# Optimization experiments

Measured on AMD Instinct MI355X. Metric: run time of the kernel, lower is better.

The kernel has to match this reference:

```python
import jax, jax.numpy as jnp
import numpy as np

N_NODES = 100000
DIM = 64
N_EDGES = 1250000
PRESERVE = 0.1  # preserve_ratio in GCN module


def gcn_conv(x, W, b, row, col, edge_w, num_nodes):
    """PyG GCNConv with normalize=True: symmetric norm with added self-loops.
    x: [N, d], W: [d, d_out], edge (row -> col) with weight edge_w: [E].
    """
    # add self-loops with weight 1
    loop = jnp.arange(num_nodes, dtype=row.dtype)
    r = jnp.concatenate([row, loop])
    c = jnp.concatenate([col, loop])
    w = jnp.concatenate([edge_w, jnp.ones((num_nodes,), dtype=edge_w.dtype)])
    # symmetric degree normalization: deg computed at target (col)
    deg = jax.ops.segment_sum(w, c, num_segments=num_nodes)
    dinv = jnp.where(deg > 0, jax.lax.rsqrt(deg), 0.0)
    norm = dinv[r] * w * dinv[c]  # [E+N]
    xw = x @ W  # [N, d_out] (linear transform before propagation)
    msg = xw[r] * norm[:, None]  # gather + scale
    out = jax.ops.segment_sum(msg, c, num_segments=num_nodes)  # scatter-add at targets
    return out + b


def setup_inputs() -> dict:
    key = jax.random.key(0)
    ks = jax.random.split(key, 8)
    skill_embed = jax.random.normal(ks[0], (N_NODES, DIM), dtype=jnp.float32)
    edge_index = jax.random.randint(ks[1], (2, N_EDGES), 0, N_NODES, dtype=jnp.int64)
    edge_attr = jax.random.uniform(ks[2], (N_EDGES,), dtype=jnp.float32)
    # GCNConv params (W stored as [in, out] here), glorot-ish init
    scale = 1.0 / np.sqrt(DIM)
    W1 = jax.random.uniform(ks[3], (DIM, DIM), minval=-scale, maxval=scale, dtype=jnp.float32)
    b1 = jnp.zeros((DIM,), dtype=jnp.float32)
    W2 = jax.random.uniform(ks[4], (DIM, DIM), minval=-scale, maxval=scale, dtype=jnp.float32)
    b2 = jnp.zeros((DIM,), dtype=jnp.float32)
    return {"skill_embed": skill_embed, "edge_index": edge_index, "edge_attr": edge_attr,
            "W1": W1, "b1": b1, "W2": W2, "b2": b2}


def reference(skill_embed, edge_index, edge_attr, W1, b1, W2, b2):
    row, col = edge_index[0], edge_index[1]
    n = skill_embed.shape[0]
    temp = skill_embed
    out = gcn_conv(skill_embed, W1, b1, row, col, edge_attr, n)
    temp = (1.0 - PRESERVE) * out + PRESERVE * temp
    out = gcn_conv(temp, W2, b2, row, col, edge_attr, n)
    temp = (1.0 - PRESERVE) * out + PRESERVE * temp
    return temp
```

## Files before the change

### kernel.cpp

```cpp
#include <hip/hip_runtime.h>

#define DIM 64
#define PRESERVE 0.1f
#define P_BLK 512
#define NBMAX 512

typedef unsigned short bf16_t;

__device__ __forceinline__ float readlane_f(float v, int l) {
    return __int_as_float(__builtin_amdgcn_readlane(__float_as_int(v), l));
}
__device__ __forceinline__ float bf2f(bf16_t u) {
    return __uint_as_float(((unsigned)u) << 16);
}
__device__ __forceinline__ bf16_t f2bf(float f) {
    unsigned u = __float_as_uint(f);
    unsigned r = (u + 0x7FFFu + ((u >> 16) & 1u)) >> 16;
    return (bf16_t)r;
}


__global__ __launch_bounds__(256) void k_bcount(const int* __restrict__ col,
                                                int* __restrict__ bh,
                                                int E, int nb, int chunk) {
    __shared__ int hist[NBMAX];
    int t = threadIdx.x;
    for (int i = t; i < nb; i += 256) hist[i] = 0;
    __syncthreads();
    int beg = blockIdx.x * chunk;
    int end = beg + chunk;
    if (end > E) end = E;
    for (int i = beg + t; i < end; i += 256) atomicAdd(&hist[col[i] >> 8], 1);
    __syncthreads();
    for (int i = t; i < nb; i += 256) bh[(size_t)i * P_BLK + blockIdx.x] = hist[i];
}

__global__ __launch_bounds__(P_BLK) void k_bscan1(int* __restrict__ bh,
                                                  int* __restrict__ btot) {
    __shared__ int s[P_BLK];
    int t = threadIdx.x;
    size_t base = (size_t)blockIdx.x * P_BLK;
    int v = bh[base + t];
    s[t] = v;
    __syncthreads();
    for (int off = 1; off < P_BLK; off <<= 1) {
        int x = (t >= off) ? s[t - off] : 0;
        __syncthreads();
        s[t] += x;
        __syncthreads();
    }
    bh[base + t] = s[t] - v;
    if (t == P_BLK - 1) btot[blockIdx.x] = s[P_BLK - 1];
}

__global__ __launch_bounds__(P_BLK) void k_bscan2(const int* __restrict__ btot,
                                                  int* __restrict__ bbase,
                                                  int nb, int E) {
    __shared__ int s[P_BLK];
    int t = threadIdx.x;
    int v = (t < nb) ? btot[t] : 0;
    s[t] = v;
    __syncthreads();
    for (int off = 1; off < P_BLK; off <<= 1) {
        int x = (t >= off) ? s[t - off] : 0;
        __syncthreads();
        s[t] += x;
        __syncthreads();
    }
    if (t < nb) bbase[t] = s[t] - v;
    if (t == 0) bbase[nb] = E;
}

__global__ __launch_bounds__(256) void k_bscatter(
        const int* __restrict__ row, const int* __restrict__ col,
        const float* __restrict__ ew, const int* __restrict__ bh,
        const int* __restrict__ bbase, int2* __restrict__ sered,
        int* __restrict__ colb, int E, int nb, int chunk) {
    __shared__ int cur[NBMAX];
    int t = threadIdx.x;
    for (int i = t; i < nb; i += 256)
        cur[i] = bbase[i] + bh[(size_t)i * P_BLK + blockIdx.x];
    __syncthreads();
    int beg = blockIdx.x * chunk;
    int end = beg + chunk;
    if (end > E) end = E;
    for (int i = beg + t; i < end; i += 256) {
        int c = col[i];
        int r = row[i];
        float w = ew[i];
        int slot = atomicAdd(&cur[c >> 8], 1);
        int2 pk;
        pk.x = r;
        pk.y = __float_as_int(w);
        sered[slot] = pk;
        colb[slot] = c;
    }
}

__global__ __launch_bounds__(256) void k_bcsr(
        const int2* __restrict__ sered, const int* __restrict__ colb,
        const int* __restrict__ bbase, int2* __restrict__ sedge,
        int* __restrict__ offsets, float* __restrict__ dinv, int N, int E) {
    __shared__ int cnt[256];
    __shared__ float degw[256];
    __shared__ int sc[256];
    __shared__ int cur[256];
    int t = threadIdx.x;
    int b = blockIdx.x;
    cnt[t] = 0;
    degw[t] = 0.0f;
    __syncthreads();
    int s0 = bbase[b];
    int e0 = bbase[b + 1];
    int nbase = b << 8;
    for (int i = s0 + t; i < e0; i += 256) {
        int loc = colb[i] - nbase;
        atomicAdd(&cnt[loc], 1);
        atomicAdd(&degw[loc], __int_as_float(sered[i].y));
    }
    __syncthreads();
    int v = cnt[t];
    sc[t] = v;
    __syncthreads();
    for (int off = 1; off < 256; off <<= 1) {
        int x = (t >= off) ? sc[t - off] : 0;
        __syncthreads();
        sc[t] += x;
        __syncthreads();
    }
    int excl = sc[t] - v;
    cur[t] = excl;
    int node = nbase + t;
    if (node < N) {
        offsets[node] = s0 + excl;
        dinv[node] = rsqrtf(1.0f + degw[t]);
    }
    if (b == 0 && t == 0) offsets[N] = E;
    __syncthreads();
    for (int i = s0 + t; i < e0; i += 256) {
        int loc = colb[i] - nbase;
        int slot = atomicAdd(&cur[loc], 1);
        sedge[s0 + slot] = sered[i];
    }
}

__global__ __launch_bounds__(256) void k_mm(
        const float* __restrict__ x, const float* __restrict__ W,
        const float* __restrict__ dinv, bf16_t* __restrict__ xs, int n) {
    int tid = threadIdx.x;
    int lane = tid & 63;
    int waveId = blockIdx.x * 4 + (tid >> 6);
    int nWaves = gridDim.x * 4;

    float Wr[DIM];
#pragma unroll
    for (int k = 0; k < DIM; ++k) Wr[k] = W[k * DIM + lane];

    for (int r0 = waveId * 4; r0 < n; r0 += nWaves * 4) {
        if (r0 + 3 < n) {
            float x0 = x[(size_t)(r0 + 0) * DIM + lane];
            float x1 = x[(size_t)(r0 + 1) * DIM + lane];
            float x2 = x[(size_t)(r0 + 2) * DIM + lane];
            float x3 = x[(size_t)(r0 + 3) * DIM + lane];
            float a0 = 0.f, a1 = 0.f, a2 = 0.f, a3 = 0.f;
#pragma unroll
            for (int k = 0; k < DIM; ++k) {
                float w = Wr[k];
                a0 += readlane_f(x0, k) * w;
                a1 += readlane_f(x1, k) * w;
                a2 += readlane_f(x2, k) * w;
                a3 += readlane_f(x3, k) * w;
            }
            xs[(size_t)(r0 + 0) * DIM + lane] = f2bf(a0 * dinv[r0 + 0]);
            xs[(size_t)(r0 + 1) * DIM + lane] = f2bf(a1 * dinv[r0 + 1]);
            xs[(size_t)(r0 + 2) * DIM + lane] = f2bf(a2 * dinv[r0 + 2]);
            xs[(size_t)(r0 + 3) * DIM + lane] = f2bf(a3 * dinv[r0 + 3]);
        } else {
            for (int r = r0; r < n; ++r) {
                float xv = x[(size_t)r * DIM + lane];
                float a = 0.f;
#pragma unroll
                for (int k = 0; k < DIM; ++k) a += readlane_f(xv, k) * Wr[k];
                xs[(size_t)r * DIM + lane] = f2bf(a * dinv[r]);
            }
        }
    }
}

__global__ __launch_bounds__(256) void k_gather(
        const bf16_t* __restrict__ xs, const int* __restrict__ offsets,
        const int2* __restrict__ sedge, const float* __restrict__ dinv,
        const float* __restrict__ b, const float* __restrict__ xprev,
        float* __restrict__ out, int n) {
    int tid = threadIdx.x;
    int lane = tid & 63;
    int c = blockIdx.x * 4 + (tid >> 6);
    if (c >= n) return;
    float di = dinv[c];
    float acc = bf2f(xs[(size_t)c * DIM + lane]);
    int beg = offsets[c];
    int end = offsets[c + 1];
    for (int b0 = beg; b0 < end; b0 += 64) {
        int m = end - b0;
        if (m > 64) m = 64;
        int r_l = 0, w_l = 0;
        if (lane < m) {
            int2 p = sedge[b0 + lane];
            r_l = p.x;
            w_l = p.y;
        }
        int j = 0;
        for (; j + 3 < m; j += 4) {
            int r0 = __builtin_amdgcn_readlane(r_l, j);
            int r1 = __builtin_amdgcn_readlane(r_l, j + 1);
            int r2 = __builtin_amdgcn_readlane(r_l, j + 2);
            int r3 = __builtin_amdgcn_readlane(r_l, j + 3);
            float w0 = readlane_f(__int_as_float(w_l), j);
            float w1 = readlane_f(__int_as_float(w_l), j + 1);
            float w2 = readlane_f(__int_as_float(w_l), j + 2);
            float w3 = readlane_f(__int_as_float(w_l), j + 3);
            float a0 = bf2f(xs[(size_t)r0 * DIM + lane]);
            float a1 = bf2f(xs[(size_t)r1 * DIM + lane]);
            float a2 = bf2f(xs[(size_t)r2 * DIM + lane]);
            float a3 = bf2f(xs[(size_t)r3 * DIM + lane]);
            acc += a0 * w0;
            acc += a1 * w1;
            acc += a2 * w2;
            acc += a3 * w3;
        }
        for (; j < m; ++j) {
            int r0 = __builtin_amdgcn_readlane(r_l, j);
            float w0 = readlane_f(__int_as_float(w_l), j);
            acc += bf2f(xs[(size_t)r0 * DIM + lane]) * w0;
        }
    }
    float v = (1.0f - PRESERVE) * (acc * di + b[lane]) + PRESERVE * xprev[(size_t)c * DIM + lane];
    out[(size_t)c * DIM + lane] = v;
}

extern "C" void kernel_launch(void* const* d_in, const int* in_sizes, int n_in,
                              void* d_out, int out_size, void* d_ws, size_t ws_size,
                              hipStream_t stream) {
    const float* x  = (const float*)d_in[0];
    const int*   ei = (const int*)d_in[1];
    const float* ew = (const float*)d_in[2];
    const float* W1 = (const float*)d_in[3];
    const float* b1 = (const float*)d_in[4];
    const float* W2 = (const float*)d_in[5];
    const float* b2 = (const float*)d_in[6];

    const int N = in_sizes[0] / DIM;
    const int E = in_sizes[2];
    const int* row = ei;
    const int* col = ei + E;

    const int nb = (N + 255) >> 8;
    const int chunk = (E + P_BLK - 1) / P_BLK;

    int2* sedge   = (int2*)d_ws;
    float* dinv   = (float*)(sedge + E);
    bf16_t* xs    = (bf16_t*)(dinv + N);
    float* temp   = (float*)(xs + (size_t)N * DIM);
    int2* sered   = (int2*)temp;
    int* colb     = (int*)(sered + E);
    int* offsets  = (int*)(temp + (size_t)N * DIM);
    int* bh       = offsets + N + 1;
    int* btot     = bh + (size_t)nb * P_BLK;
    int* bbase    = btot + nb;

    const int B = 256;
    const int nblkG = (N + 3) / 4;
    const int nblkMM = 1024;

    k_bcount<<<P_BLK, B, 0, stream>>>(col, bh, E, nb, chunk);
    k_bscan1<<<nb, P_BLK, 0, stream>>>(bh, btot);
    k_bscan2<<<1, P_BLK, 0, stream>>>(btot, bbase, nb, E);
    k_bscatter<<<P_BLK, B, 0, stream>>>(row, col, ew, bh, bbase, sered, colb,
                                        E, nb, chunk);
    k_bcsr<<<nb, B, 0, stream>>>(sered, colb, bbase, sedge, offsets, dinv, N, E);

    k_mm<<<nblkMM, B, 0, stream>>>(x, W1, dinv, xs, N);
    k_gather<<<nblkG, B, 0, stream>>>(xs, offsets, sedge, dinv, b1, x, temp, N);

    k_mm<<<nblkMM, B, 0, stream>>>(temp, W2, dinv, xs, N);
    k_gather<<<nblkG, B, 0, stream>>>(xs, offsets, sedge, dinv, b2, temp, (float*)d_out, N);
}
```

Measured before the change: 297.1 us.

## Replace per-node CSR sort with 64-node buckets and LDS-atomic gather

```diff
diff --git a/kernel.cpp b/kernel.cpp
--- a/kernel.cpp
+++ b/kernel.cpp
@@ -2,8 +2,12 @@
 
 #define DIM 64
 #define PRESERVE 0.1f
-#define P_BLK 512
-#define NBMAX 512
+#define P_BLK 1024
+#define BSH 6
+#define BNODES 64
+#define NBMAX 2048
+#define ROWB 20
+#define ROWM ((1 << ROWB) - 1)
 
 typedef unsigned short bf16_t;
 
@@ -30,117 +34,106 @@
     int beg = blockIdx.x * chunk;
     int end = beg + chunk;
     if (end > E) end = E;
-    for (int i = beg + t; i < end; i += 256) atomicAdd(&hist[col[i] >> 8], 1);
-    __syncthreads();
-    for (int i = t; i < nb; i += 256) bh[(size_t)i * P_BLK + blockIdx.x] = hist[i];
-}
-
-__global__ __launch_bounds__(P_BLK) void k_bscan1(int* __restrict__ bh,
-                                                  int* __restrict__ btot) {
-    __shared__ int s[P_BLK];
-    int t = threadIdx.x;
-    size_t base = (size_t)blockIdx.x * P_BLK;
-    int v = bh[base + t];
-    s[t] = v;
-    __syncthreads();
-    for (int off = 1; off < P_BLK; off <<= 1) {
+    for (int i = beg + t; i < end; i += 256) atomicAdd(&hist[col[i] >> BSH], 1);
+    __syncthreads();
+    size_t base = (size_t)blockIdx.x * nb;
+    for (int i = t; i < nb; i += 256) bh[base + i] = hist[i];
+}
+
+__global__ __launch_bounds__(256) void k_bscan1(const int* __restrict__ bh,
+                                                int* __restrict__ bh2,
+                                                int* __restrict__ btot, int nb) {
+    __shared__ int s[256];
+    int t = threadIdx.x;
+    int i = blockIdx.x;
+    int v0 = bh[(size_t)(t * 4 + 0) * nb + i];
+    int v1 = bh[(size_t)(t * 4 + 1) * nb + i];
+    int v2 = bh[(size_t)(t * 4 + 2) * nb + i];
+    int v3 = bh[(size_t)(t * 4 + 3) * nb + i];
+    int sum = v0 + v1 + v2 + v3;
+    s[t] = sum;
+    __syncthreads();
+    for (int off = 1; off < 256; off <<= 1) {
         int x = (t >= off) ? s[t - off] : 0;
         __syncthreads();
         s[t] += x;
         __syncthreads();
     }
-    bh[base + t] = s[t] - v;
-    if (t == P_BLK - 1) btot[blockIdx.x] = s[P_BLK - 1];
-}
-
-__global__ __launch_bounds__(P_BLK) void k_bscan2(const int* __restrict__ btot,
-                                                  int* __restrict__ bbase,
-                                                  int nb, int E) {
-    __shared__ int s[P_BLK];
-    int t = threadIdx.x;
-    int v = (t < nb) ? btot[t] : 0;
-    s[t] = v;
-    __syncthreads();
-    for (int off = 1; off < P_BLK; off <<= 1) {
+    int run = s[t] - sum;
+    size_t ob = (size_t)i * P_BLK + t * 4;
+    bh2[ob + 0] = run; run += v0;
+    bh2[ob + 1] = run; run += v1;
+    bh2[ob + 2] = run; run += v2;
+    bh2[ob + 3] = run;
+    if (t == 255) btot[i] = s[255];
+}
+
+__global__ __launch_bounds__(1024) void k_bscan2(const int* __restrict__ btot,
+                                                 int* __restrict__ bbase,
+                                                 int nb, int E) {
+    __shared__ int s[1024];
+    int t = threadIdx.x;
+    int a0 = (2 * t < nb) ? btot[2 * t] : 0;
+    int a1 = (2 * t + 1 < nb) ? btot[2 * t + 1] : 0;
+    int sum = a0 + a1;
+    s[t] = sum;
+    __syncthreads();
+    for (int off = 1; off < 1024; off <<= 1) {
         int x = (t >= off) ? s[t - off] : 0;
         __syncthreads();
         s[t] += x;
         __syncthreads();
     }
-    if (t < nb) bbase[t] = s[t] - v;
+    int excl = s[t] - sum;
+    if (2 * t < nb) bbase[2 * t] = excl;
+    if (2 * t + 1 < nb) bbase[2 * t + 1] = excl + a0;
     if (t == 0) bbase[nb] = E;
 }
 
 __global__ __launch_bounds__(256) void k_bscatter(
         const int* __restrict__ row, const int* __restrict__ col,
-        const float* __restrict__ ew, const int* __restrict__ bh,
+        const float* __restrict__ ew, const int* __restrict__ bh2,
         const int* __restrict__ bbase, int2* __restrict__ sered,
-        int* __restrict__ colb, int E, int nb, int chunk) {
+        int E, int nb, int chunk) {
     __shared__ int cur[NBMAX];
     int t = threadIdx.x;
+    int blk = blockIdx.x;
     for (int i = t; i < nb; i += 256)
-        cur[i] = bbase[i] + bh[(size_t)i * P_BLK + blockIdx.x];
-    __syncthreads();
-    int beg = blockIdx.x * chunk;
+        cur[i] = bbase[i] + bh2[(size_t)i * P_BLK + blk];
+    __syncthreads();
+    int beg = blk * chunk;
     int end = beg + chunk;
     if (end > E) end = E;
     for (int i = beg + t; i < end; i += 256) {
         int c = col[i];
         int r = row[i];
         float w = ew[i];
-        int slot = atomicAdd(&cur[c >> 8], 1);
-        int2 pk;
-        pk.x = r;
-        pk.y = __float_as_int(w);
-        sered[slot] = pk;
-        colb[slot] = c;
-    }
-}
-
-__global__ __launch_bounds__(256) void k_bcsr(
-        const int2* __restrict__ sered, const int* __restrict__ colb,
-        const int* __restrict__ bbase, int2* __restrict__ sedge,
-        int* __restrict__ offsets, float* __restrict__ dinv, int N, int E) {
-    __shared__ int cnt[256];
-    __shared__ float degw[256];
-    __shared__ int sc[256];
-    __shared__ int cur[256];
+        int slot = atomicAdd(&cur[c >> BSH], 1);
+        int2 p;
+        p.x = r | ((c & (BNODES - 1)) << ROWB);
+        p.y = __float_as_int(w);
+        sered[slot] = p;
+    }
+}
+
+__global__ __launch_bounds__(256) void k_bdeg(const int2* __restrict__ sered,
+                                              const int* __restrict__ bbase,
+                                              float* __restrict__ dinv, int N) {
+    __shared__ float deg[BNODES];
     int t = threadIdx.x;
     int b = blockIdx.x;
-    cnt[t] = 0;
-    degw[t] = 0.0f;
+    if (t < BNODES) deg[t] = 0.0f;
     __syncthreads();
     int s0 = bbase[b];
     int e0 = bbase[b + 1];
-    int nbase = b << 8;
     for (int i = s0 + t; i < e0; i += 256) {
-        int loc = colb[i] - nbase;
-        atomicAdd(&cnt[loc], 1);
-        atomicAdd(&degw[loc], __int_as_float(sered[i].y));
-    }
-    __syncthreads();
-    int v = cnt[t];
-    sc[t] = v;
-    __syncthreads();
-    for (int off = 1; off < 256; off <<= 1) {
-        int x = (t >= off) ? sc[t - off] : 0;
-        __syncthreads();
-        sc[t] += x;
-        __syncthreads();
-    }
-    int excl = sc[t] - v;
-    cur[t] = excl;
-    int node = nbase + t;
-    if (node < N) {
-        offsets[node] = s0 + excl;
-        dinv[node] = rsqrtf(1.0f + degw[t]);
-    }
-    if (b == 0 && t == 0) offsets[N] = E;
-    __syncthreads();
-    for (int i = s0 + t; i < e0; i += 256) {
-        int loc = colb[i] - nbase;
-        int slot = atomicAdd(&cur[loc], 1);
-        sedge[s0 + slot] = sered[i];
+        int2 p = sered[i];
+        atomicAdd(&deg[((unsigned)p.x) >> ROWB], __int_as_float(p.y));
+    }
+    __syncthreads();
+    if (t < BNODES) {
+        int node = (b << BSH) + t;
+        if (node < N) dinv[node] = rsqrtf(1.0f + deg[t]);
     }
 }
 
@@ -187,55 +180,72 @@
     }
 }
 
-__global__ __launch_bounds__(256) void k_gather(
-        const bf16_t* __restrict__ xs, const int* __restrict__ offsets,
-        const int2* __restrict__ sedge, const float* __restrict__ dinv,
-        const float* __restrict__ b, const float* __restrict__ xprev,
-        float* __restrict__ out, int n) {
-    int tid = threadIdx.x;
-    int lane = tid & 63;
-    int c = blockIdx.x * 4 + (tid >> 6);
-    if (c >= n) return;
-    float di = dinv[c];
-    float acc = bf2f(xs[(size_t)c * DIM + lane]);
-    int beg = offsets[c];
-    int end = offsets[c + 1];
-    for (int b0 = beg; b0 < end; b0 += 64) {
-        int m = end - b0;
+__global__ __launch_bounds__(256) void k_bgather(
+        const bf16_t* __restrict__ xs, const int2* __restrict__ sered,
+        const int* __restrict__ bbase, const float* __restrict__ dinv,
+        const float* __restrict__ bias, const float* __restrict__ xprev,
+        float* __restrict__ out, int N) {
+    __shared__ float acc[BNODES * DIM];
+    int t = threadIdx.x;
+    int lane = t & 63;
+    int wid = t >> 6;
+    int b = blockIdx.x;
+    int nbase = b << BSH;
+
+    for (int i = wid; i < BNODES; i += 4) {
+        int node = nbase + i;
+        acc[i * DIM + lane] = (node < N) ? bf2f(xs[(size_t)node * DIM + lane]) : 0.0f;
+    }
+    __syncthreads();
+
+    int s0 = bbase[b];
+    int e0 = bbase[b + 1];
+    for (int b0 = s0 + wid * 64; b0 < e0; b0 += 256) {
+        int m = e0 - b0;
         if (m > 64) m = 64;
-        int r_l = 0, w_l = 0;
+        int kl = 0, wl = 0;
         if (lane < m) {
-            int2 p = sedge[b0 + lane];
-            r_l = p.x;
-            w_l = p.y;
+            int2 p = sered[b0 + lane];
+            kl = p.x;
+            wl = p.y;
         }
         int j = 0;
         for (; j + 3 < m; j += 4) {
-            int r0 = __builtin_amdgcn_readlane(r_l, j);
-            int r1 = __builtin_amdgcn_readlane(r_l, j + 1);
-            int r2 = __builtin_amdgcn_readlane(r_l, j + 2);
-            int r3 = __builtin_amdgcn_readlane(r_l, j + 3);
-            float w0 = readlane_f(__int_as_float(w_l), j);
-            float w1 = readlane_f(__int_as_float(w_l), j + 1);
-            float w2 = readlane_f(__int_as_float(w_l), j + 2);
-            float w3 = readlane_f(__int_as_float(w_l), j + 3);
-            float a0 = bf2f(xs[(size_t)r0 * DIM + lane]);
-            float a1 = bf2f(xs[(size_t)r1 * DIM + lane]);
-            float a2 = bf2f(xs[(size_t)r2 * DIM + lane]);
-            float a3 = bf2f(xs[(size_t)r3 * DIM + lane]);
-            acc += a0 * w0;
-            acc += a1 * w1;
-            acc += a2 * w2;
-            acc += a3 * w3;
+            int k0 = __builtin_amdgcn_readlane(kl, j);
+            int k1 = __builtin_amdgcn_readlane(kl, j + 1);
+            int k2 = __builtin_amdgcn_readlane(kl, j + 2);
+            int k3 = __builtin_amdgcn_readlane(kl, j + 3);
+            float w0 = readlane_f(__int_as_float(wl), j);
+            float w1 = readlane_f(__int_as_float(wl), j + 1);
+            float w2 = readlane_f(__int_as_float(wl), j + 2);
+            float w3 = readlane_f(__int_as_float(wl), j + 3);
+            float a0 = bf2f(xs[(size_t)(k0 & ROWM) * DIM + lane]);
+            float a1 = bf2f(xs[(size_t)(k1 & ROWM) * DIM + lane]);
+            float a2 = bf2f(xs[(size_t)(k2 & ROWM) * DIM + lane]);
+            float a3 = bf2f(xs[(size_t)(k3 & ROWM) * DIM + lane]);
+            atomicAdd(&acc[(((unsigned)k0) >> ROWB) * DIM + lane], a0 * w0);
+            atomicAdd(&acc[(((unsigned)k1) >> ROWB) * DIM + lane], a1 * w1);
+            atomicAdd(&acc[(((unsigned)k2) >> ROWB) * DIM + lane], a2 * w2);
+            atomicAdd(&acc[(((unsigned)k3) >> ROWB) * DIM + lane], a3 * w3);
         }
         for (; j < m; ++j) {
-            int r0 = __builtin_amdgcn_readlane(r_l, j);
-            float w0 = readlane_f(__int_as_float(w_l), j);
-            acc += bf2f(xs[(size_t)r0 * DIM + lane]) * w0;
-        }
-    }
-    float v = (1.0f - PRESERVE) * (acc * di + b[lane]) + PRESERVE * xprev[(size_t)c * DIM + lane];
-    out[(size_t)c * DIM + lane] = v;
+            int k0 = __builtin_amdgcn_readlane(kl, j);
+            float w0 = readlane_f(__int_as_float(wl), j);
+            float a0 = bf2f(xs[(size_t)(k0 & ROWM) * DIM + lane]);
+            atomicAdd(&acc[(((unsigned)k0) >> ROWB) * DIM + lane], a0 * w0);
+        }
+    }
+    __syncthreads();
+
+    float bl = bias[lane];
+    for (int i = wid; i < BNODES; i += 4) {
+        int node = nbase + i;
+        if (node < N) {
+            float v = (1.0f - PRESERVE) * (acc[i * DIM + lane] * dinv[node] + bl)
+                    + PRESERVE * xprev[(size_t)node * DIM + lane];
+            out[(size_t)node * DIM + lane] = v;
+        }
+    }
 }
 
 extern "C" void kernel_launch(void* const* d_in, const int* in_sizes, int n_in,
@@ -254,34 +264,30 @@
     const int* row = ei;
     const int* col = ei + E;
 
-    const int nb = (N + 255) >> 8;
+    const int nb = (N + BNODES - 1) >> BSH;
     const int chunk = (E + P_BLK - 1) / P_BLK;
 
-    int2* sedge   = (int2*)d_ws;
-    float* dinv   = (float*)(sedge + E);
+    int2* sered   = (int2*)d_ws;
+    float* dinv   = (float*)(sered + E);
     bf16_t* xs    = (bf16_t*)(dinv + N);
-    float* temp   = (float*)(xs + (size_t)N * DIM);
-    int2* sered   = (int2*)temp;
-    int* colb     = (int*)(sered + E);
-    int* offsets  = (int*)(temp + (size_t)N * DIM);
-    int* bh       = offsets + N + 1;
-    int* btot     = bh + (size_t)nb * P_BLK;
+    int* btot     = (int*)(xs + (size_t)N * DIM);
     int* bbase    = btot + nb;
+    float* temp   = (float*)(bbase + nb + 1);
+    int* bh       = (int*)temp;
+    int* bh2      = bh + (size_t)P_BLK * nb;
 
     const int B = 256;
-    const int nblkG = (N + 3) / 4;
     const int nblkMM = 1024;
 
     k_bcount<<<P_BLK, B, 0, stream>>>(col, bh, E, nb, chunk);
-    k_bscan1<<<nb, P_BLK, 0, stream>>>(bh, btot);
-    k_bscan2<<<1, P_BLK, 0, stream>>>(btot, bbase, nb, E);
-    k_bscatter<<<P_BLK, B, 0, stream>>>(row, col, ew, bh, bbase, sered, colb,
-                                        E, nb, chunk);
-    k_bcsr<<<nb, B, 0, stream>>>(sered, colb, bbase, sedge, offsets, dinv, N, E);
+    k_bscan1<<<nb, B, 0, stream>>>(bh, bh2, btot, nb);
+    k_bscan2<<<1, 1024, 0, stream>>>(btot, bbase, nb, E);
+    k_bscatter<<<P_BLK, B, 0, stream>>>(row, col, ew, bh2, bbase, sered, E, nb, chunk);
+    k_bdeg<<<nb, B, 0, stream>>>(sered, bbase, dinv, N);
 
     k_mm<<<nblkMM, B, 0, stream>>>(x, W1, dinv, xs, N);
-    k_gather<<<nblkG, B, 0, stream>>>(xs, offsets, sedge, dinv, b1, x, temp, N);
+    k_bgather<<<nb, B, 0, stream>>>(xs, sered, bbase, dinv, b1, x, temp, N);
 
     k_mm<<<nblkMM, B, 0, stream>>>(temp, W2, dinv, xs, N);
-    k_gather<<<nblkG, B, 0, stream>>>(xs, offsets, sedge, dinv, b2, temp, (float*)d_out, N);
-}
+    k_bgather<<<nb, B, 0, stream>>>(xs, sered, bbase, dinv, b2, temp, (float*)d_out, N);
+}
```

After: 1.149 ms. +286.6%, slower.
